# Optimization experiments

Hardware: AMD Instinct MI355X
Metric: run time of the kernel (lower is better)

## Reference

```python
import jax, jax.numpy as jnp
import numpy as np

DIM = 512
HEADS = 8
HEAD_DIM = DIM // HEADS
R = 2  # reduce_ratio
SCALE = HEAD_DIM ** -0.5


def setup_inputs() -> dict:
    key = jax.random.key(0)
    ks = jax.random.split(key, 8)
    bs, H, W = 4, 64, 64
    n = H * W
    std = 0.02
    x = jax.random.normal(ks[0], (bs, n, DIM), dtype=jnp.float32)
    q_w = jax.random.normal(ks[1], (DIM, DIM), dtype=jnp.float32) * std
    kv_w = jax.random.normal(ks[2], (DIM, 2 * DIM), dtype=jnp.float32) * std
    proj_w = jax.random.normal(ks[3], (DIM, DIM), dtype=jnp.float32) * std
    proj_b = jnp.zeros((DIM,), dtype=jnp.float32)
    # Conv2d(dim, dim, kernel=R, stride=R), kaiming-like init
    fan_out = R * R * DIM
    sr_w = jax.random.normal(ks[4], (DIM, DIM, R, R), dtype=jnp.float32) * np.sqrt(2.0 / fan_out)
    sr_b = jnp.zeros((DIM,), dtype=jnp.float32)
    ln_w = jnp.ones((DIM,), dtype=jnp.float32)
    ln_b = jnp.zeros((DIM,), dtype=jnp.float32)
    return {"x": x, "q_w": q_w, "kv_w": kv_w, "proj_w": proj_w, "proj_b": proj_b,
            "sr_w": sr_w, "sr_b": sr_b, "ln_w": ln_w, "ln_b": ln_b, "H": H, "W": W}


def _layernorm(x, w, b, eps=1e-5):
    mu = jnp.mean(x, axis=-1, keepdims=True)
    var = jnp.var(x, axis=-1, keepdims=True)
    return (x - mu) * jax.lax.rsqrt(var + eps) * w + b


def reference(x, q_w, kv_w, proj_w, proj_b, sr_w, sr_b, ln_w, ln_b, H, W):
    bs, n, ch = x.shape
    # q: (bs, heads, n, head_dim)
    q = (x @ q_w).reshape(bs, n, HEADS, HEAD_DIM).transpose(0, 2, 1, 3)
    # spatial reduction of kv source: strided conv + layernorm
    x_img = x.transpose(0, 2, 1).reshape(bs, ch, H, W)
    xr = jax.lax.conv_general_dilated(
        x_img, sr_w, window_strides=(R, R), padding='VALID',
        dimension_numbers=('NCHW', 'OIHW', 'NCHW')) + sr_b[None, :, None, None]
    xr = xr.reshape(bs, ch, -1).transpose(0, 2, 1)  # (bs, n_kv, ch)
    xr = _layernorm(xr, ln_w, ln_b)
    kv = xr @ kv_w  # (bs, n_kv, 2*ch)
    n_kv = kv.shape[1]
    kv = kv.reshape(bs, n_kv, 2, HEADS, HEAD_DIM).transpose(2, 0, 3, 1, 4)
    k, v = kv[0], kv[1]  # (bs, heads, n_kv, head_dim)
    att = jnp.einsum('bhqd,bhkd->bhqk', q, k) * SCALE
    att = jax.nn.softmax(att, axis=-1)
    net = jnp.einsum('bhqk,bhkd->bhqd', att, v)
    net = net.transpose(0, 2, 1, 3).reshape(bs, n, ch)
    return net @ proj_w + proj_b
```

## Files before the change

kernel.cpp:

```cpp
#include <hip/hip_runtime.h>
#include <cstdint>

#define HEADS 8
#define HD 64
#define NQ 4096
#define NKV 1024

typedef unsigned short u16;
typedef __attribute__((ext_vector_type(8))) short short8;
typedef __attribute__((ext_vector_type(4))) float f32x4;
typedef __attribute__((ext_vector_type(16))) float f32x16;

__device__ __forceinline__ u16 f2bf(float f){
  union { float f; unsigned u; } c; c.f = f;
  unsigned r = c.u + 0x7fffu + ((c.u >> 16) & 1u);
  return (u16)(r >> 16);
}
__device__ __forceinline__ unsigned pack2(float a, float b){
  return (unsigned)f2bf(a) | ((unsigned)f2bf(b) << 16);
}
__device__ __forceinline__ float fexp2(float x){
  float r;
  asm("v_exp_f32 %0, %1" : "=v"(r) : "v"(x));
  return r;
}
__device__ __forceinline__ unsigned cvtpk(float a, float b){
  unsigned r;
  asm("v_cvt_pk_bf16_f32 %0, %1, %2" : "=v"(r) : "v"(a), "v"(b));
  return r;
}
__device__ __forceinline__ void gll16(const void* g, void* l){
  __builtin_amdgcn_global_load_lds((const __attribute__((address_space(1))) unsigned*)g,
                                   (__attribute__((address_space(3))) unsigned*)l, 16, 0, 0);
}
#define SB0() __builtin_amdgcn_sched_barrier(0)
#define MFMA16(a, b, c) __builtin_amdgcn_mfma_f32_16x16x32_bf16(a, b, c, 0, 0, 0)
#define MFMA32(a, b, c) __builtin_amdgcn_mfma_f32_32x32x16_bf16(a, b, c, 0, 0, 0)
#define Z16 {0.f,0.f,0.f,0.f,0.f,0.f,0.f,0.f,0.f,0.f,0.f,0.f,0.f,0.f,0.f,0.f}

__global__ __launch_bounds__(256) void prep_all(const float* __restrict__ x,
                                                const float* __restrict__ q_w,
                                                const float* __restrict__ kv_w,
                                                const float* __restrict__ proj_w,
                                                const float* __restrict__ sr_w,
                                                u16* __restrict__ x_bf,
                                                u16* __restrict__ q_wT, u16* __restrict__ kv_wT,
                                                u16* __restrict__ proj_wT, u16* __restrict__ conv_BT){
  int bid = blockIdx.x;
  if (bid < 4096){
    int tid = bid * 256 + threadIdx.x;
    size_t src = (size_t)tid * 8;
    const float4* s4 = (const float4*)(x + src);
    float4 v0 = s4[0], v1 = s4[1];
    uint4 p;
    p.x = pack2(v0.x, v0.y); p.y = pack2(v0.z, v0.w);
    p.z = pack2(v1.x, v1.y); p.w = pack2(v1.z, v1.w);
    *(uint4*)(x_bf + src) = p;
    return;
  }
  int e = (bid - 4096) * 256 + threadIdx.x;
  if (e < 262144){ int n = e >> 9, k = e & 511; q_wT[e] = f2bf(q_w[k * 512 + n]); return; }
  e -= 262144;
  if (e < 524288){ int n = e >> 9, k = e & 511; kv_wT[e] = f2bf(kv_w[k * 1024 + n]); return; }
  e -= 524288;
  if (e < 262144){ int n = e >> 9, k = e & 511; proj_wT[e] = f2bf(proj_w[k * 512 + n]); return; }
  e -= 262144;
  { int co = e >> 11, r = e & 2047, t = r >> 9, ci = r & 511;
    conv_BT[e] = f2bf(sr_w[co * 2048 + ci * 4 + t]); }
}

__global__ __launch_bounds__(256) void gemm_qconv(const u16* __restrict__ x_bf, const u16* __restrict__ q_wT,
                                                  const u16* __restrict__ conv_BT,
                                                  u16* __restrict__ q_sb, float* __restrict__ xr_pre,
                                                  const float* __restrict__ sr_b){
  __shared__ __align__(16) u16 As[128 * 64];
  __shared__ __align__(16) u16 Bs[128 * 64];
  const int tid = threadIdx.x, lane = tid & 63, wave = tid >> 6;
  const int l15 = lane & 15, g = lane >> 4, r7 = l15 & 7;
  const int wr = wave >> 1, wc = wave & 1;
  int y = blockIdx.y;
  const bool isQ = (y >= 64);
  int kz = 0, m0, kb = 0, iters, KB;
  const u16* BT;
  if (isQ){ m0 = (y - 64) * 128; iters = 8;  KB = 512;  BT = q_wT; }
  else { kz = y >> 5; m0 = (y & 31) * 128; kb = kz << 10; iters = 16; KB = 2048; BT = conv_BT; }
  const int n0 = blockIdx.x * 128;

  unsigned aBase[4], bBase[4];
  #pragma unroll
  for (int ii = 0; ii < 4; ++ii){
    int c = ii * 256 + tid;
    int row = c >> 3, sc = (c & 7) ^ (row & 7);
    if (isQ) aBase[ii] = (unsigned)(m0 + row) * 512 + sc * 8;
    else { int grow = m0 + row, b = grow >> 10, pr = grow & 1023;
           aBase[ii] = ((unsigned)(b * 4096) + (pr >> 5) * 128 + (pr & 31) * 2) * 512 + sc * 8; }
    bBase[ii] = (unsigned)(n0 + row) * KB + sc * 8;
  }

  f32x4 acc[4][4] = {};
  for (int i = 0; i < iters; ++i){
    int kt = kb + i * 64;
    unsigned aOff;
    if (isQ) aOff = kt;
    else { int t = kt >> 9; aOff = (unsigned)((t >> 1) * 64 + (t & 1)) * 512 + (kt & 511); }
    #pragma unroll
    for (int ii = 0; ii < 4; ++ii){
      gll16(x_bf + aBase[ii] + aOff, As + (size_t)(ii * 256 + wave * 64) * 8);
      gll16(BT + bBase[ii] + kt,     Bs + (size_t)(ii * 256 + wave * 64) * 8);
    }
    __syncthreads();
    #pragma unroll
    for (int kk = 0; kk < 2; ++kk){
      short8 af[4];
      #pragma unroll
      for (int mi = 0; mi < 4; ++mi)
        af[mi] = *(const short8*)(As + (wr * 64 + mi * 16 + l15) * 64 + (((kk * 4 + g) ^ r7) << 3));
      #pragma unroll
      for (int ni = 0; ni < 4; ++ni){
        short8 bf = *(const short8*)(Bs + (wc * 64 + ni * 16 + l15) * 64 + (((kk * 4 + g) ^ r7) << 3));
        #pragma unroll
        for (int mi = 0; mi < 4; ++mi)
          acc[mi][ni] = MFMA16(af[mi], bf, acc[mi][ni]);
      }
    }
    __syncthreads();
  }
  #pragma unroll
  for (int mi = 0; mi < 4; ++mi){
    int row = m0 + wr * 64 + mi * 16 + (lane >> 4) * 4;
    #pragma unroll
    for (int ni = 0; ni < 4; ++ni){
      int col = n0 + wc * 64 + ni * 16 + l15;
      f32x4 v = acc[mi][ni];
      if (isQ){
        int h = col >> 6, d = col & 63;
        #pragma unroll
        for (int j = 0; j < 4; ++j){
          int r = row + j, b = r >> 12, nq = r & 4095;
          q_sb[(((size_t)(b * HEADS + h)) * NQ + nq) * HD + d] = f2bf(v[j] * 0.18033688f);
        }
      } else {
        float* Co = xr_pre + (size_t)kz * 4096 * 512;
        float bb = (kz == 0) ? sr_b[col] : 0.f;
        #pragma unroll
        for (int j = 0; j < 4; ++j) Co[(size_t)(row + j) * 512 + col] = v[j] + bb;
      }
    }
  }
}

__global__ __launch_bounds__(256) void gemm_kv(const u16* __restrict__ A, const u16* __restrict__ BT,
                                               u16* __restrict__ Cb0, u16* __restrict__ Cb1){
  __shared__ __align__(16) u16 As[64 * 64];
  __shared__ __align__(16) u16 Bs[128 * 64];
  const int tid = threadIdx.x, lane = tid & 63, wave = tid >> 6;
  const int l15 = lane & 15, g = lane >> 4, r7 = l15 & 7;
  const int m0 = blockIdx.y * 64, n0 = blockIdx.x * 128;
  const int wr = wave >> 1, wc = wave & 1;
  f32x4 acc[2][4] = {};
  for (int kt = 0; kt < 512; kt += 64){
    #pragma unroll
    for (int i = 0; i < 2; ++i){
      int c = i * 256 + tid;
      int row = c >> 3, sc = (c & 7) ^ (row & 7);
      gll16(A + (size_t)(m0 + row) * 512 + kt + sc * 8, As + (size_t)(i * 256 + wave * 64) * 8);
    }
    #pragma unroll
    for (int i = 0; i < 4; ++i){
      int c = i * 256 + tid;
      int row = c >> 3, sc = (c & 7) ^ (row & 7);
      gll16(BT + (size_t)(n0 + row) * 512 + kt + sc * 8, Bs + (size_t)(i * 256 + wave * 64) * 8);
    }
    __syncthreads();
    #pragma unroll
    for (int kk = 0; kk < 2; ++kk){
      short8 af[2];
      #pragma unroll
      for (int mi = 0; mi < 2; ++mi)
        af[mi] = *(const short8*)(As + (wr * 32 + mi * 16 + l15) * 64 + (((kk * 4 + g) ^ r7) << 3));
      #pragma unroll
      for (int ni = 0; ni < 4; ++ni){
        short8 bf = *(const short8*)(Bs + (wc * 64 + ni * 16 + l15) * 64 + (((kk * 4 + g) ^ r7) << 3));
        #pragma unroll
        for (int mi = 0; mi < 2; ++mi)
          acc[mi][ni] = MFMA16(af[mi], bf, acc[mi][ni]);
      }
    }
    __syncthreads();
  }
  #pragma unroll
  for (int mi = 0; mi < 2; ++mi){
    int row = m0 + wr * 32 + mi * 16 + (lane >> 4) * 4;
    #pragma unroll
    for (int ni = 0; ni < 4; ++ni){
      int col = n0 + wc * 64 + ni * 16 + l15;
      f32x4 v = acc[mi][ni];
      int s = col >> 9, h = (col >> 6) & 7, d = col & 63;
      if (s == 0){
        #pragma unroll
        for (int j = 0; j < 4; ++j){
          int r = row + j, b = r >> 10, p = r & 1023;
          Cb0[(((size_t)(b * HEADS + h)) * NKV + p) * HD + d] = f2bf(v[j]);
        }
      } else {
        int b = row >> 10, p0 = row & 1023;
        int pp = (p0 & ~12) | (((p0 >> 2) & 1) << 3) | (((p0 >> 3) & 1) << 2);
        ushort4 pk;
        pk.x = f2bf(v[0]); pk.y = f2bf(v[1]); pk.z = f2bf(v[2]); pk.w = f2bf(v[3]);
        *(ushort4*)(Cb1 + (((size_t)(b * HEADS + h)) * HD + d) * NKV + pp) = pk;
      }
    }
  }
}

__global__ __launch_bounds__(256) void gemm_proj(const u16* __restrict__ A, const u16* __restrict__ BT,
                                                 float* __restrict__ Cf, const float* __restrict__ bias,
                                                 int M, int N, int K){
  __shared__ __align__(16) u16 As[128 * 64];
  __shared__ __align__(16) u16 Bs[128 * 64];
  const int tid = threadIdx.x, lane = tid & 63, wave = tid >> 6;
  const int l15 = lane & 15, g = lane >> 4, r7 = l15 & 7;
  const int m0 = blockIdx.y * 128, n0 = blockIdx.x * 128;
  const int wr = wave >> 1, wc = wave & 1;
  f32x4 acc[4][4] = {};
  for (int kt = 0; kt < K; kt += 64){
    #pragma unroll
    for (int i = 0; i < 4; ++i){
      int c = i * 256 + tid;
      int row = c >> 3, sc = (c & 7) ^ (row & 7);
      gll16(A  + (size_t)(m0 + row) * K + kt + sc * 8, As + (size_t)(i * 256 + wave * 64) * 8);
      gll16(BT + (size_t)(n0 + row) * K + kt + sc * 8, Bs + (size_t)(i * 256 + wave * 64) * 8);
    }
    __syncthreads();
    #pragma unroll
    for (int kk = 0; kk < 2; ++kk){
      short8 af[4];
      #pragma unroll
      for (int mi = 0; mi < 4; ++mi)
        af[mi] = *(const short8*)(As + (wr * 64 + mi * 16 + l15) * 64 + (((kk * 4 + g) ^ r7) << 3));
      #pragma unroll
      for (int ni = 0; ni < 4; ++ni){
        short8 bf = *(const short8*)(Bs + (wc * 64 + ni * 16 + l15) * 64 + (((kk * 4 + g) ^ r7) << 3));
        #pragma unroll
        for (int mi = 0; mi < 4; ++mi)
          acc[mi][ni] = MFMA16(af[mi], bf, acc[mi][ni]);
      }
    }
    __syncthreads();
  }
  #pragma unroll
  for (int mi = 0; mi < 4; ++mi){
    int row = m0 + wr * 64 + mi * 16 + (lane >> 4) * 4;
    #pragma unroll
    for (int ni = 0; ni < 4; ++ni){
      int col = n0 + wc * 64 + ni * 16 + l15;
      f32x4 v = acc[mi][ni];
      float bb = bias[col];
      #pragma unroll
      for (int j = 0; j < 4; ++j) Cf[(size_t)(row + j) * N + col] = v[j] + bb;
    }
  }
}

__global__ __launch_bounds__(256) void ln_k(const float* __restrict__ xp,
                                            const float* __restrict__ w,
                                            const float* __restrict__ bias, u16* __restrict__ xr){
  int row = blockIdx.x * 4 + (threadIdx.x >> 6);
  int lane = threadIdx.x & 63;
  const float* s1 = xp + (size_t)row * 512;
  const float* s2 = s1 + (size_t)4096 * 512;
  float vals[8]; float s = 0.f, ss = 0.f;
  #pragma unroll
  for (int j = 0; j < 8; ++j){
    int c = lane + j * 64;
    float v = s1[c] + s2[c];
    vals[j] = v; s += v; ss += v * v;
  }
  #pragma unroll
  for (int off = 32; off >= 1; off >>= 1){ s += __shfl_xor(s, off); ss += __shfl_xor(ss, off); }
  float mean = s * (1.f / 512.f);
  float var  = ss * (1.f / 512.f) - mean * mean;
  float rs = rsqrtf(var + 1e-5f);
  u16* dst = xr + (size_t)row * 512;
  #pragma unroll
  for (int j = 0; j < 8; ++j){
    int c = lane + j * 64;
    dst[c] = f2bf((vals[j] - mean) * rs * w[c] + bias[c]);
  }
}

template<bool LAST>
__device__ __forceinline__ void attn_tile(const u16* ksb, const u16* vsb,
                                          u16* kstage, u16* vstage,
                                          const u16* akg, const u16* avg,
                                          const short8* qf,
                                          int l31, int hi, int x7,
                                          f32x16* o, float& l_run){
  asm volatile("s_waitcnt vmcnt(0)" ::: "memory");
  __builtin_amdgcn_s_barrier();
  SB0();

  unsigned w[16];
  float ps = 0.f;

  f32x16 a0 = Z16;
  __builtin_amdgcn_s_setprio(1);
  #pragma unroll
  for (int ks = 0; ks < 4; ++ks){
    short8 kf = *(const short8*)(ksb + l31 * 64 + (((ks * 2 + hi) ^ x7) << 3));
    a0 = MFMA32(kf, qf[ks], a0);
  }
  __builtin_amdgcn_s_setprio(0);

  if (!LAST){
    gll16(akg,              kstage);
    gll16(akg + 2048,       kstage + 2048);
    gll16(avg,              vstage);
    gll16(avg + 32 * 1024,  vstage + 2048);
  }

  #pragma unroll
  for (int t = 0; t < 8; ++t){
    float p0 = fexp2(a0[2 * t]), p1 = fexp2(a0[2 * t + 1]);
    ps += p0 + p1;
    w[t] = cvtpk(p0, p1);
  }

  {
    f32x16 a = Z16;
    __builtin_amdgcn_s_setprio(1);
    #pragma unroll
    for (int ks = 0; ks < 4; ++ks){
      short8 kf = *(const short8*)(ksb + (32 + l31) * 64 + (((ks * 2 + hi) ^ x7) << 3));
      a = MFMA32(kf, qf[ks], a);
    }
    __builtin_amdgcn_s_setprio(0);
    #pragma unroll
    for (int t = 0; t < 8; ++t){
      float p0 = fexp2(a[2 * t]), p1 = fexp2(a[2 * t + 1]);
      ps += p0 + p1;
      w[8 + t] = cvtpk(p0, p1);
    }
  }
  l_run += ps;

  __builtin_amdgcn_s_setprio(1);
  #pragma unroll
  for (int sl = 0; sl < 4; ++sl){
    union { unsigned u[4]; short8 s; } bb;
    bb.u[0] = w[sl * 4 + 0]; bb.u[1] = w[sl * 4 + 1];
    bb.u[2] = w[sl * 4 + 2]; bb.u[3] = w[sl * 4 + 3];
    #pragma unroll
    for (int dt = 0; dt < 2; ++dt){
      short8 vf = *(const short8*)(vsb + (dt * 32 + l31) * 64 + (((sl * 2 + hi) ^ x7) << 3));
      o[dt] = MFMA32(vf, bb.s, o[dt]);
    }
  }
  __builtin_amdgcn_s_setprio(0);
}

__global__ __launch_bounds__(256) void attn_k(const u16* __restrict__ q_s, const u16* __restrict__ k_s,
                                              const u16* __restrict__ vt_s, u16* __restrict__ net){
  __shared__ __align__(16) u16 Ks[2][64 * 64];
  __shared__ __align__(16) u16 Vt[2][64 * 64];
  const int tid = threadIdx.x, lane = tid & 63, wave = tid >> 6;
  const int l31 = lane & 31, hi = lane >> 5, x7 = lane & 7;
  const int id = blockIdx.x;
  const int xcd = id & 7, slot = id >> 3;
  const int bh = 4 * xcd + (slot >> 5);
  const int qblk = slot & 31;
  const u16* kb  = k_s  + (size_t)bh * NKV * HD;
  const u16* vtb = vt_s + (size_t)bh * HD * NKV;
  const int q0 = qblk * 128 + wave * 32;
  const u16* qbase = q_s + ((size_t)bh * NQ + q0 + l31) * HD + hi * 8;
  short8 qf[4];
  #pragma unroll
  for (int ks = 0; ks < 4; ++ks) qf[ks] = *(const short8*)(qbase + ks * 16);

  const int swz8 = (((tid & 7) ^ ((tid >> 3) & 7)) << 3);
  const u16* ak0 = kb  + (size_t)(tid >> 3) * 64   + swz8;
  const u16* av0 = vtb + (size_t)(tid >> 3) * 1024 + swz8;

  f32x16 o[2] = { Z16, Z16 };
  float l_run = 0.f;

  gll16(ak0,             &Ks[0][wave * 512]);
  gll16(ak0 + 2048,      &Ks[0][2048 + wave * 512]);
  gll16(av0,             &Vt[0][wave * 512]);
  gll16(av0 + 32 * 1024, &Vt[0][2048 + wave * 512]);

  for (int tt = 0; tt < 7; ++tt){
    attn_tile<false>(&Ks[0][0], &Vt[0][0], &Ks[1][wave * 512], &Vt[1][wave * 512],
                     ak0 + (size_t)(2 * tt + 1) * 4096, av0 + (2 * tt + 1) * 64,
                     qf, l31, hi, x7, o, l_run);
    attn_tile<false>(&Ks[1][0], &Vt[1][0], &Ks[0][wave * 512], &Vt[0][wave * 512],
                     ak0 + (size_t)(2 * tt + 2) * 4096, av0 + (2 * tt + 2) * 64,
                     qf, l31, hi, x7, o, l_run);
  }
  attn_tile<false>(&Ks[0][0], &Vt[0][0], &Ks[1][wave * 512], &Vt[1][wave * 512],
                   ak0 + (size_t)15 * 4096, av0 + 15 * 64,
                   qf, l31, hi, x7, o, l_run);
  attn_tile<true>(&Ks[1][0], &Vt[1][0], nullptr, nullptr, nullptr, nullptr,
                  qf, l31, hi, x7, o, l_run);

  float l = l_run + __shfl_xor(l_run, 32);
  float inv = 1.f / l;
  int b = bh >> 3, h = bh & 7;
  size_t obase = ((size_t)b * NQ + q0 + l31) * 512 + h * 64;
  #pragma unroll
  for (int dt = 0; dt < 2; ++dt)
    #pragma unroll
    for (int t = 0; t < 8; ++t){
      int j = 2 * t;
      int d = dt * 32 + (j & 3) + 8 * (j >> 2) + 4 * hi;
      *(unsigned*)(net + obase + d) = cvtpk(o[dt][j] * inv, o[dt][j + 1] * inv);
    }
}

extern "C" void kernel_launch(void* const* d_in, const int* in_sizes, int n_in,
                              void* d_out, int out_size, void* d_ws, size_t ws_size,
                              hipStream_t stream){
  const float* x      = (const float*)d_in[0];
  const float* q_w    = (const float*)d_in[1];
  const float* kv_w   = (const float*)d_in[2];
  const float* proj_w = (const float*)d_in[3];
  const float* proj_b = (const float*)d_in[4];
  const float* sr_w   = (const float*)d_in[5];
  const float* sr_b   = (const float*)d_in[6];
  const float* ln_w   = (const float*)d_in[7];
  const float* ln_b   = (const float*)d_in[8];
  (void)in_sizes; (void)n_in; (void)out_size; (void)ws_size;

  char* ws = (char*)d_ws;
  u16*   x_bf    = (u16*)(ws);
  u16*   xr      = (u16*)(ws + ((size_t)16 << 20));
  u16*   net     = (u16*)(ws + ((size_t)16 << 20));
  u16*   q_sb    = (u16*)(ws + ((size_t)32 << 20));
  float* xr_pre  = (float*)(ws + ((size_t)48 << 20));
  u16*   k_sb    = (u16*)(ws + ((size_t)48 << 20));
  u16*   vt_sb   = (u16*)(ws + ((size_t)52 << 20));
  u16*   q_wT    = (u16*)(ws + ((size_t)64 << 20));
  u16*   kv_wT   = (u16*)(ws + ((size_t)64 << 20) + 524288);
  u16*   proj_wT = (u16*)(ws + ((size_t)64 << 20) + 524288 + 1048576);
  u16*   conv_BT = (u16*)(ws + ((size_t)64 << 20) + 524288 + 1048576 + 524288);
  float* out = (float*)d_out;

  prep_all<<<12288, 256, 0, stream>>>(x, q_w, kv_w, proj_w, sr_w,
                                      x_bf, q_wT, kv_wT, proj_wT, conv_BT);
  gemm_qconv<<<dim3(4, 192), 256, 0, stream>>>(x_bf, q_wT, conv_BT, q_sb, xr_pre, sr_b);
  ln_k<<<1024, 256, 0, stream>>>(xr_pre, ln_w, ln_b, xr);
  gemm_kv<<<dim3(8, 64), 256, 0, stream>>>(xr, kv_wT, k_sb, vt_sb);
  attn_k<<<1024, 256, 0, stream>>>(q_sb, k_sb, vt_sb, net);
  gemm_proj<<<dim3(4, 128), 256, 0, stream>>>(net, proj_wT, out, proj_b, 16384, 512, 512);
}
```

Measured before the change: 131.7 us.

## Process two query sub-tiles per wave in attention, halve block size

The attention kernel now gives each wave 64 query rows as two 32-row sub-tiles, so every K and V fragment read from LDS feeds two MFMAs. Blocks shrink from 4 waves to 2 while each block still covers 128 queries, and each thread issues 8 cooperative global-to-LDS loads per tile instead of 4. The PV product is split into two halves to keep the P fragments small. The goal is to cut LDS read traffic and barrier cost per MFMA, at the price of roughly double the accumulator and Q registers, fewer waves to hide latency, and more load work per thread.

```diff
diff --git a/kernel.cpp b/kernel.cpp
--- a/kernel.cpp
+++ b/kernel.cpp
@@ -293,73 +293,99 @@
 __device__ __forceinline__ void attn_tile(const u16* ksb, const u16* vsb,
                                           u16* kstage, u16* vstage,
                                           const u16* akg, const u16* avg,
-                                          const short8* qf,
+                                          const short8* qfA, const short8* qfB,
                                           int l31, int hi, int x7,
-                                          f32x16* o, float& l_run){
+                                          f32x16* oA, f32x16* oB,
+                                          float& lA, float& lB){
   asm volatile("s_waitcnt vmcnt(0)" ::: "memory");
   __builtin_amdgcn_s_barrier();
   SB0();
 
-  unsigned w[16];
-  float ps = 0.f;
-
-  f32x16 a0 = Z16;
+  unsigned wA[8], wB[8];
+  float psA = 0.f, psB = 0.f;
+
+  {
+    f32x16 aA = Z16, aB = Z16;
+    __builtin_amdgcn_s_setprio(1);
+    #pragma unroll
+    for (int ks = 0; ks < 4; ++ks){
+      short8 kf = *(const short8*)(ksb + l31 * 64 + (((ks * 2 + hi) ^ x7) << 3));
+      aA = MFMA32(kf, qfA[ks], aA);
+      aB = MFMA32(kf, qfB[ks], aB);
+    }
+    __builtin_amdgcn_s_setprio(0);
+
+    if (!LAST){
+      #pragma unroll
+      for (int j = 0; j < 4; ++j){
+        gll16(akg + j * 1024,  kstage + j * 1024);
+        gll16(avg + j * 16384, vstage + j * 1024);
+      }
+    }
+
+    #pragma unroll
+    for (int t = 0; t < 8; ++t){
+      float a0 = fexp2(aA[2 * t]), a1 = fexp2(aA[2 * t + 1]);
+      psA += a0 + a1; wA[t] = cvtpk(a0, a1);
+      float b0 = fexp2(aB[2 * t]), b1 = fexp2(aB[2 * t + 1]);
+      psB += b0 + b1; wB[t] = cvtpk(b0, b1);
+    }
+  }
   __builtin_amdgcn_s_setprio(1);
   #pragma unroll
-  for (int ks = 0; ks < 4; ++ks){
-    short8 kf = *(const short8*)(ksb + l31 * 64 + (((ks * 2 + hi) ^ x7) << 3));
-    a0 = MFMA32(kf, qf[ks], a0);
+  for (int sl = 0; sl < 2; ++sl){
+    union { unsigned u[4]; short8 s; } bA, bB;
+    bA.u[0] = wA[sl * 4 + 0]; bA.u[1] = wA[sl * 4 + 1];
+    bA.u[2] = wA[sl * 4 + 2]; bA.u[3] = wA[sl * 4 + 3];
+    bB.u[0] = wB[sl * 4 + 0]; bB.u[1] = wB[sl * 4 + 1];
+    bB.u[2] = wB[sl * 4 + 2]; bB.u[3] = wB[sl * 4 + 3];
+    #pragma unroll
+    for (int dt = 0; dt < 2; ++dt){
+      short8 vf = *(const short8*)(vsb + (dt * 32 + l31) * 64 + (((sl * 2 + hi) ^ x7) << 3));
+      oA[dt] = MFMA32(vf, bA.s, oA[dt]);
+      oB[dt] = MFMA32(vf, bB.s, oB[dt]);
+    }
   }
   __builtin_amdgcn_s_setprio(0);
 
-  if (!LAST){
-    gll16(akg,              kstage);
-    gll16(akg + 2048,       kstage + 2048);
-    gll16(avg,              vstage);
-    gll16(avg + 32 * 1024,  vstage + 2048);
-  }
-
-  #pragma unroll
-  for (int t = 0; t < 8; ++t){
-    float p0 = fexp2(a0[2 * t]), p1 = fexp2(a0[2 * t + 1]);
-    ps += p0 + p1;
-    w[t] = cvtpk(p0, p1);
-  }
-
   {
-    f32x16 a = Z16;
+    f32x16 aA = Z16, aB = Z16;
     __builtin_amdgcn_s_setprio(1);
     #pragma unroll
     for (int ks = 0; ks < 4; ++ks){
       short8 kf = *(const short8*)(ksb + (32 + l31) * 64 + (((ks * 2 + hi) ^ x7) << 3));
-      a = MFMA32(kf, qf[ks], a);
+      aA = MFMA32(kf, qfA[ks], aA);
+      aB = MFMA32(kf, qfB[ks], aB);
     }
     __builtin_amdgcn_s_setprio(0);
     #pragma unroll
     for (int t = 0; t < 8; ++t){
-      float p0 = fexp2(a[2 * t]), p1 = fexp2(a[2 * t + 1]);
-      ps += p0 + p1;
-      w[8 + t] = cvtpk(p0, p1);
-    }
-  }
-  l_run += ps;
-
+      float a0 = fexp2(aA[2 * t]), a1 = fexp2(aA[2 * t + 1]);
+      psA += a0 + a1; wA[t] = cvtpk(a0, a1);
+      float b0 = fexp2(aB[2 * t]), b1 = fexp2(aB[2 * t + 1]);
+      psB += b0 + b1; wB[t] = cvtpk(b0, b1);
+    }
+  }
+  lA += psA; lB += psB;
   __builtin_amdgcn_s_setprio(1);
   #pragma unroll
-  for (int sl = 0; sl < 4; ++sl){
-    union { unsigned u[4]; short8 s; } bb;
-    bb.u[0] = w[sl * 4 + 0]; bb.u[1] = w[sl * 4 + 1];
-    bb.u[2] = w[sl * 4 + 2]; bb.u[3] = w[sl * 4 + 3];
+  for (int sl = 2; sl < 4; ++sl){
+    union { unsigned u[4]; short8 s; } bA, bB;
+    bA.u[0] = wA[(sl - 2) * 4 + 0]; bA.u[1] = wA[(sl - 2) * 4 + 1];
+    bA.u[2] = wA[(sl - 2) * 4 + 2]; bA.u[3] = wA[(sl - 2) * 4 + 3];
+    bB.u[0] = wB[(sl - 2) * 4 + 0]; bB.u[1] = wB[(sl - 2) * 4 + 1];
+    bB.u[2] = wB[(sl - 2) * 4 + 2]; bB.u[3] = wB[(sl - 2) * 4 + 3];
     #pragma unroll
     for (int dt = 0; dt < 2; ++dt){
       short8 vf = *(const short8*)(vsb + (dt * 32 + l31) * 64 + (((sl * 2 + hi) ^ x7) << 3));
-      o[dt] = MFMA32(vf, bb.s, o[dt]);
+      oA[dt] = MFMA32(vf, bA.s, oA[dt]);
+      oB[dt] = MFMA32(vf, bB.s, oB[dt]);
     }
   }
   __builtin_amdgcn_s_setprio(0);
 }
 
-__global__ __launch_bounds__(256) void attn_k(const u16* __restrict__ q_s, const u16* __restrict__ k_s,
+__global__ __launch_bounds__(128) void attn_k(const u16* __restrict__ q_s, const u16* __restrict__ k_s,
                                               const u16* __restrict__ vt_s, u16* __restrict__ net){
   __shared__ __align__(16) u16 Ks[2][64 * 64];
   __shared__ __align__(16) u16 Vt[2][64 * 64];
@@ -371,49 +397,61 @@
   const int qblk = slot & 31;
   const u16* kb  = k_s  + (size_t)bh * NKV * HD;
   const u16* vtb = vt_s + (size_t)bh * HD * NKV;
-  const int q0 = qblk * 128 + wave * 32;
+  const int q0 = qblk * 128 + wave * 64;
   const u16* qbase = q_s + ((size_t)bh * NQ + q0 + l31) * HD + hi * 8;
-  short8 qf[4];
-  #pragma unroll
-  for (int ks = 0; ks < 4; ++ks) qf[ks] = *(const short8*)(qbase + ks * 16);
+  short8 qfA[4], qfB[4];
+  #pragma unroll
+  for (int ks = 0; ks < 4; ++ks){
+    qfA[ks] = *(const short8*)(qbase + ks * 16);
+    qfB[ks] = *(const short8*)(qbase + 32 * HD + ks * 16);
+  }
 
   const int swz8 = (((tid & 7) ^ ((tid >> 3) & 7)) << 3);
   const u16* ak0 = kb  + (size_t)(tid >> 3) * 64   + swz8;
   const u16* av0 = vtb + (size_t)(tid >> 3) * 1024 + swz8;
 
-  f32x16 o[2] = { Z16, Z16 };
-  float l_run = 0.f;
-
-  gll16(ak0,             &Ks[0][wave * 512]);
-  gll16(ak0 + 2048,      &Ks[0][2048 + wave * 512]);
-  gll16(av0,             &Vt[0][wave * 512]);
-  gll16(av0 + 32 * 1024, &Vt[0][2048 + wave * 512]);
+  f32x16 oA[2] = { Z16, Z16 }, oB[2] = { Z16, Z16 };
+  float lA = 0.f, lB = 0.f;
+
+  u16* k0 = &Ks[0][wave * 512];
+  u16* v0 = &Vt[0][wave * 512];
+  u16* k1 = &Ks[1][wave * 512];
+  u16* v1 = &Vt[1][wave * 512];
+
+  #pragma unroll
+  for (int j = 0; j < 4; ++j){
+    gll16(ak0 + j * 1024,  k0 + j * 1024);
+    gll16(av0 + j * 16384, v0 + j * 1024);
+  }
 
   for (int tt = 0; tt < 7; ++tt){
-    attn_tile<false>(&Ks[0][0], &Vt[0][0], &Ks[1][wave * 512], &Vt[1][wave * 512],
+    attn_tile<false>(&Ks[0][0], &Vt[0][0], k1, v1,
                      ak0 + (size_t)(2 * tt + 1) * 4096, av0 + (2 * tt + 1) * 64,
-                     qf, l31, hi, x7, o, l_run);
-    attn_tile<false>(&Ks[1][0], &Vt[1][0], &Ks[0][wave * 512], &Vt[0][wave * 512],
+                     qfA, qfB, l31, hi, x7, oA, oB, lA, lB);
+    attn_tile<false>(&Ks[1][0], &Vt[1][0], k0, v0,
                      ak0 + (size_t)(2 * tt + 2) * 4096, av0 + (2 * tt + 2) * 64,
-                     qf, l31, hi, x7, o, l_run);
-  }
-  attn_tile<false>(&Ks[0][0], &Vt[0][0], &Ks[1][wave * 512], &Vt[1][wave * 512],
+                     qfA, qfB, l31, hi, x7, oA, oB, lA, lB);
+  }
+  attn_tile<false>(&Ks[0][0], &Vt[0][0], k1, v1,
                    ak0 + (size_t)15 * 4096, av0 + 15 * 64,
-                   qf, l31, hi, x7, o, l_run);
+                   qfA, qfB, l31, hi, x7, oA, oB, lA, lB);
   attn_tile<true>(&Ks[1][0], &Vt[1][0], nullptr, nullptr, nullptr, nullptr,
-                  qf, l31, hi, x7, o, l_run);
-
-  float l = l_run + __shfl_xor(l_run, 32);
-  float inv = 1.f / l;
+                  qfA, qfB, l31, hi, x7, oA, oB, lA, lB);
+
+  float ltA = lA + __shfl_xor(lA, 32);
+  float ltB = lB + __shfl_xor(lB, 32);
+  float invA = 1.f / ltA, invB = 1.f / ltB;
   int b = bh >> 3, h = bh & 7;
-  size_t obase = ((size_t)b * NQ + q0 + l31) * 512 + h * 64;
+  size_t obaseA = ((size_t)b * NQ + q0 + l31) * 512 + h * 64;
+  size_t obaseB = obaseA + (size_t)32 * 512;
   #pragma unroll
   for (int dt = 0; dt < 2; ++dt)
     #pragma unroll
     for (int t = 0; t < 8; ++t){
       int j = 2 * t;
       int d = dt * 32 + (j & 3) + 8 * (j >> 2) + 4 * hi;
-      *(unsigned*)(net + obase + d) = cvtpk(o[dt][j] * inv, o[dt][j + 1] * inv);
+      *(unsigned*)(net + obaseA + d) = cvtpk(oA[dt][j] * invA, oA[dt][j + 1] * invA);
+      *(unsigned*)(net + obaseB + d) = cvtpk(oB[dt][j] * invB, oB[dt][j + 1] * invB);
     }
 }
 
@@ -450,6 +488,6 @@
   gemm_qconv<<<dim3(4, 192), 256, 0, stream>>>(x_bf, q_wT, conv_BT, q_sb, xr_pre, sr_b);
   ln_k<<<1024, 256, 0, stream>>>(xr_pre, ln_w, ln_b, xr);
   gemm_kv<<<dim3(8, 64), 256, 0, stream>>>(xr, kv_wT, k_sb, vt_sb);
-  attn_k<<<1024, 256, 0, stream>>>(q_sb, k_sb, vt_sb, net);
+  attn_k<<<1024, 128, 0, stream>>>(q_sb, k_sb, vt_sb, net);
   gemm_proj<<<dim3(4, 128), 256, 0, stream>>>(net, proj_wT, out, proj_b, 16384, 512, 512);
 }
```

Result: no change. 131.4 us (median of 3 runs) (-0.3%).
